# Performance work log

Hardware: AMD Instinct MI355X
Metric: run time of the kernel (lower is better)

Reference implementation:

```python
import jax, jax.numpy as jnp
import numpy as np

NTYPES = 2
B, N, MNEI = 4, 512, 100
M = MNEI * NTYPES          # neighbor slots = maxNeighborNum * ntypes
EMB_LAST = 100             # embedding net sizes [25, 50, 100]
FIT_H = 240
M2 = 16
RMIN, RMAX = 0.5, 6.0


def setup_inputs():
    key = jax.random.key(0)
    ks = jax.random.split(key, 24)
    r = jax.random.uniform(ks[0], (B, N, M), minval=0.6, maxval=7.0)
    v = jax.random.normal(ks[1], (B, N, M, 3))
    v = v / jnp.linalg.norm(v, axis=-1, keepdims=True)
    keep = jax.random.uniform(ks[2], (B, N, M)) < 0.7
    ImageDR = jnp.concatenate([r[..., None], r[..., None] * v], axis=-1)
    ImageDR = jnp.where(keep[..., None], ImageDR, 0.0).astype(jnp.float32)
    Imagetype_map = jax.random.randint(ks[3], (N,), 0, NTYPES)
    list_neigh = jax.random.randint(ks[4], (B, N, M), 0, N + 1)
    type_map = jnp.arange(NTYPES)
    davg = (0.01 * jax.random.normal(ks[5], (NTYPES, M, 4))).astype(jnp.float32)
    dstd = (1.0 + 0.1 * jax.random.uniform(ks[6], (NTYPES, M, 4))).astype(jnp.float32)

    def w(k, shape, fan):
        return (jax.random.normal(k, shape) / np.sqrt(fan)).astype(jnp.float32)

    def b(k, shape):
        return (0.1 * jax.random.normal(k, shape)).astype(jnp.float32)

    emb_W0 = w(ks[7], (NTYPES, NTYPES, 1, 25), 1)
    emb_b0 = b(ks[8], (NTYPES, NTYPES, 25))
    emb_W1 = w(ks[9], (NTYPES, NTYPES, 25, 50), 25)
    emb_b1 = b(ks[10], (NTYPES, NTYPES, 50))
    emb_W2 = w(ks[11], (NTYPES, NTYPES, 50, 100), 50)
    emb_b2 = b(ks[12], (NTYPES, NTYPES, 100))
    fin = M2 * EMB_LAST
    fit_W0 = w(ks[13], (NTYPES, fin, FIT_H), fin)
    fit_b0 = b(ks[14], (NTYPES, FIT_H))
    fit_W1 = w(ks[15], (NTYPES, FIT_H, FIT_H), FIT_H)
    fit_b1 = b(ks[16], (NTYPES, FIT_H))
    fit_W2 = w(ks[17], (NTYPES, FIT_H, FIT_H), FIT_H)
    fit_b2 = b(ks[18], (NTYPES, FIT_H))
    fit_W3 = w(ks[19], (NTYPES, FIT_H, 1), FIT_H)
    fit_b3 = b(ks[20], (NTYPES, 1))
    energy_shift = jnp.array([-3.37, -5.21], dtype=jnp.float32)
    return dict(list_neigh=list_neigh, Imagetype_map=Imagetype_map, type_map=type_map,
                ImageDR=ImageDR, nghost=0, davg=davg, dstd=dstd,
                emb_W0=emb_W0, emb_b0=emb_b0, emb_W1=emb_W1, emb_b1=emb_b1,
                emb_W2=emb_W2, emb_b2=emb_b2,
                fit_W0=fit_W0, fit_b0=fit_b0, fit_W1=fit_W1, fit_b1=fit_b1,
                fit_W2=fit_W2, fit_b2=fit_b2, fit_W3=fit_W3, fit_b3=fit_b3,
                energy_shift=energy_shift)


def _emb(s, W0, b0, W1, b1, W2, b2):
    # DeepPot-SE embedding net with doubling resnet connections
    h = jnp.tanh(s @ W0 + b0)                                   # [..., 25]
    h = jnp.tanh(h @ W1 + b1) + jnp.concatenate([h, h], -1)     # [..., 50]
    return jnp.tanh(h @ W2 + b2) + jnp.concatenate([h, h], -1)  # [..., 100]


def _fit(d, W0, b0, W1, b1, W2, b2, W3, b3):
    h = jnp.tanh(d @ W0 + b0)
    h = h + jnp.tanh(h @ W1 + b1)
    h = h + jnp.tanh(h @ W2 + b2)
    return h @ W3 + b3


def _forward(ImageDR, davg, dstd,
             emb_W0, emb_b0, emb_W1, emb_b1, emb_W2, emb_b2,
             fit_W0, fit_b0, fit_W1, fit_b1, fit_W2, fit_b2, fit_W3, fit_b3,
             energy_shift, Imagetype_map):
    Bsz, Nat, Mtot, _ = ImageDR.shape
    m = Mtot // NTYPES
    R = ImageDR[..., 0]
    Rsafe = jnp.where(R > 1e-5, R, 1.0)
    # smooth switching function s(r): 1/r below Rmin, polynomial taper to Rmax
    u = (R - RMIN) / (RMAX - RMIN)
    mid = (u ** 3 * (-6.0 * u * u + 15.0 * u - 10.0) + 1.0) / Rsafe
    S = jnp.where((R > 0) & (R < RMIN), 1.0 / Rsafe,
                  jnp.where((R > RMIN) & (R < RMAX), mid, 0.0))
    msk = (jnp.abs(R) > 1e-5)[..., None]
    Ri = jnp.concatenate([S[..., None],
                          jnp.where(msk, (S / Rsafe)[..., None] * ImageDR[..., 1:4], 0.0)],
                         axis=-1)                                    # [B,N,M,4] = (s, s*x/r, s*y/r, s*z/r)
    # per-center-type normalization (irregular gather of stats)
    Rn = (Ri - davg[Imagetype_map][None]) / dstd[Imagetype_map][None]
    tmask = [(Imagetype_map == i).astype(Rn.dtype)[None, :, None, None] for i in range(NTYPES)]
    xyz = jnp.zeros((Bsz, Nat, 4, EMB_LAST), Rn.dtype)
    for j in range(NTYPES):                                          # neighbor-type slice
        sl = Rn[:, :, j * m:(j + 1) * m, :]                          # [B,N,m,4]
        s = sl[..., 0:1]
        G = jnp.zeros(sl.shape[:3] + (EMB_LAST,), sl.dtype)
        for i in range(NTYPES):                                      # center type -> pair net (i, j)
            G = G + tmask[i] * _emb(s, emb_W0[i, j], emb_b0[i, j],
                                    emb_W1[i, j], emb_b1[i, j], emb_W2[i, j], emb_b2[i, j])
        xyz = xyz + jnp.einsum('bnmk,bnmc->bnkc', sl, G)
    xyz = xyz / (m * NTYPES)
    # descriptor D = (Ri^T G)^T (Ri^T G)[:, :M2], flattened -> [B,N,EMB_LAST*M2]
    D = jnp.einsum('bnkc,bnkd->bncd', xyz, xyz[..., :M2]).reshape(Bsz, Nat, -1)
    Ei = jnp.zeros((Bsz, Nat), D.dtype)
    for i in range(NTYPES):
        e = _fit(D, fit_W0[i], fit_b0[i], fit_W1[i], fit_b1[i],
                 fit_W2[i], fit_b2[i], fit_W3[i], fit_b3[i])[..., 0] + energy_shift[i]
        Ei = Ei + tmask[i][:, :, 0, 0] * e
    Etot = jnp.sum(Ei, axis=1)
    return Etot, Ei


def reference(list_neigh, Imagetype_map, type_map, ImageDR, nghost, davg, dstd,
              emb_W0, emb_b0, emb_W1, emb_b1, emb_W2, emb_b2,
              fit_W0, fit_b0, fit_W1, fit_b1, fit_W2, fit_b2, fit_W3, fit_b3,
              energy_shift):
    return _forward(ImageDR, davg, dstd,
                    emb_W0, emb_b0, emb_W1, emb_b1, emb_W2, emb_b2,
                    fit_W0, fit_b0, fit_W1, fit_b1, fit_W2, fit_b2, fit_W3, fit_b3,
                    energy_shift, Imagetype_map)
```

## Files before the change

### kernel.cpp

```cpp
#include <hip/hip_runtime.h>
#include <math.h>

#define NT 2
#define BSZ 4
#define NAT 512
#define NATOMS 2048
#define NNEI 200
#define EMB 100
#define FITH 240
#define DDIM 1600
#define TBK 1024

#define BIAS_F  16
#define W3C_F   (BIAS_F + 3 * 512)
#define PERM_I  2064
#define CNT_I   (PERM_I + 2064)
#define IPERM_I (CNT_I + 4)
#define USH_BYTE 24832
#define TBL_U   0
#define W0T_U   409600
#define W1T_U   (W0T_U + 819200)
#define W2T_U   (W1T_U + 262144)
#define D_U     (W2T_U + 262144)
#define D_SZ    (129 * 50 * 512)
#define USH_END (D_U + D_SZ)
#define WS_NEED ((size_t)USH_BYTE + (size_t)USH_END * 2)

#define N_W0 819200
#define N_W1 262144
#define N_W2 262144
#define N_B  1536
#define N_W3 512
#define N_EI 2048
#define N_WT (N_W0 + N_W1 + N_W2 + N_B + N_W3 + N_EI)
#define WT_BLK ((N_WT + 255) / 256)
#define TB_BLK 512

#define HPAD 264

typedef short s8v __attribute__((ext_vector_type(8)));
typedef float f4v __attribute__((ext_vector_type(4)));

__device__ __forceinline__ float ftanh(float x) {
    float ax = fabsf(x);
    float e = __expf(2.0f * ax);
    float t = 1.0f - __fdividef(2.0f, e + 1.0f);
    return (x < 0.0f) ? -t : t;
}
__device__ __forceinline__ unsigned short f2bf(float f) {
    unsigned u = __float_as_uint(f);
    u += 0x7FFFu + ((u >> 16) & 1u);
    return (unsigned short)(u >> 16);
}
__device__ __forceinline__ float bf2f(unsigned short s) {
    return __uint_as_float(((unsigned)s) << 16);
}
__device__ __forceinline__ float calc_S(float R) {
    float Rsafe = (R > 1e-5f) ? R : 1.0f;
    float u = (R - 0.5f) * (1.0f / 5.5f);
    float uu = u * u;
    float mid = (u * uu * (-6.0f * uu + 15.0f * u - 10.0f) + 1.0f) / Rsafe;
    float S = 0.0f;
    if (R > 0.0f && R < 0.5f)      S = 1.0f / Rsafe;
    else if (R > 0.5f && R < 6.0f) S = mid;
    return S;
}

__global__ void __launch_bounds__(256) prep_kernel(
    const float* __restrict__ fW0, const float* __restrict__ fW1,
    const float* __restrict__ fW2,
    const float* __restrict__ fb0, const float* __restrict__ fb1,
    const float* __restrict__ fb2,
    const float* __restrict__ fW3, const float* __restrict__ fb3,
    const float* __restrict__ eshift,
    const float* __restrict__ davg, const float* __restrict__ dstd,
    const float* __restrict__ eW0, const float* __restrict__ eb0,
    const float* __restrict__ eW1, const float* __restrict__ eb1,
    const float* __restrict__ eW2, const float* __restrict__ eb2,
    const int* __restrict__ itype,
    float* __restrict__ ws, float* __restrict__ out)
{
    __shared__ float los[100], his[100];
    __shared__ float rng[2];
    __shared__ float h0s[8][25];
    __shared__ float h1s[8][50];
    __shared__ int pcnt, poff0, poff1;
    const int tid = threadIdx.x;
    int bxg = blockIdx.x;
    unsigned short* u0 = (unsigned short*)((char*)ws + USH_BYTE);

    if (bxg < WT_BLK) {
        int id = bxg * 256 + tid;
        if (id < N_W0) {
            int e = id & 7, lane = (id >> 3) & 63;
            int rem = id >> 9;
            int kt = rem % 50, c16 = rem / 50;
            int n = c16 * 16 + (lane & 15);
            int k = kt * 32 + (lane >> 4) * 8 + e;
            float v = 0.0f;
            if (n < 240)                  v = fW0[(size_t)k * 240 + n];
            else if (n >= 256 && n < 496) v = fW0[(size_t)(1600 + k) * 240 + (n - 256)];
            u0[W0T_U + id] = f2bf(v);
            return;
        }
        id -= N_W0;
        if (id < N_W1) {
            int e = id & 7, lane = (id >> 3) & 63;
            int rem = id >> 9;
            int kt = rem & 15, c16 = rem >> 4;
            int n = c16 * 16 + (lane & 15);
            int k = kt * 32 + (lane >> 4) * 8 + e;
            float v = 0.0f;
            if (n < 240 && k < 240)       v = fW1[(size_t)k * 240 + n];
            else if (n >= 256 && n < 496 && k >= 256 && k < 496)
                                          v = fW1[(size_t)(240 + (k - 256)) * 240 + (n - 256)];
            u0[W1T_U + id] = f2bf(v);
            return;
        }
        id -= N_W1;
        if (id < N_W2) {
            int e = id & 7, lane = (id >> 3) & 63;
            int rem = id >> 9;
            int kt = rem & 15, c16 = rem >> 4;
            int n = c16 * 16 + (lane & 15);
            int k = kt * 32 + (lane >> 4) * 8 + e;
            float v = 0.0f;
            if (n < 240 && k < 240)       v = fW2[(size_t)k * 240 + n];
            else if (n >= 256 && n < 496 && k >= 256 && k < 496)
                                          v = fW2[(size_t)(240 + (k - 256)) * 240 + (n - 256)];
            u0[W2T_U + id] = f2bf(v);
            return;
        }
        id -= N_W2;
        if (id < N_B) {
            int l = id / 512, n = id - l * 512;
            const float* fb = (l == 0) ? fb0 : (l == 1) ? fb1 : fb2;
            float v = 0.0f;
            if (n < 240)                  v = fb[n];
            else if (n >= 256 && n < 496) v = fb[240 + (n - 256)];
            ws[BIAS_F + l * 512 + n] = v;
            return;
        }
        id -= N_B;
        if (id < N_W3) {
            int n = id;
            float v = 0.0f;
            if (n < 240)                  v = fW3[n];
            else if (n >= 256 && n < 496) v = fW3[240 + (n - 256)];
            ws[W3C_F + n] = v;
            return;
        }
        id -= N_W3;
        if (id < N_EI) {
            int t = itype[id & (NAT - 1)];
            out[4 + id] = fb3[t] + eshift[t];
        }
        return;
    }
    bxg -= WT_BLK;
    if (bxg < TB_BLK) {
        const int nid = bxg >> 7;
        const int kb  = (bxg & 127) * 8;
        const int t = nid >> 1, j = nid & 1;
        if (tid < 100) {
            int m = j * 100 + tid;
            float av = davg[(t * NNEI + m) * 4];
            float sd = dstd[(t * NNEI + m) * 4];
            float inv = __fdividef(1.0f, sd);
            float a = (0.0f - av) * inv;
            float b = (2.0f - av) * inv;
            los[tid] = fminf(a, b);
            his[tid] = fmaxf(a, b);
        }
        __syncthreads();
        if (tid == 0) {
            float lo = los[0], hi = his[0];
            for (int i = 1; i < 100; ++i) { lo = fminf(lo, los[i]); hi = fmaxf(hi, his[i]); }
            rng[0] = lo; rng[1] = hi - lo;
            if (kb == 0) {
                ws[nid * 2] = lo;
                ws[nid * 2 + 1] = (float)(TBK - 1) / (hi - lo);
            }
        }
        __syncthreads();
        const float smin = rng[0], span = rng[1];
        const float* W0 = eW0 + nid * 25;
        const float* B0 = eb0 + nid * 25;
        if (tid < 200) {
            int q = tid / 25, a = tid % 25;
            float s = smin + span * ((float)(kb + q) * (1.0f / (TBK - 1)));
            h0s[q][a] = ftanh(fmaf(s, W0[a], B0[a]));
        }
        __syncthreads();
        const float* W1 = eW1 + nid * 1250;
        const float* B1 = eb1 + nid * 50;
        for (int idx = tid; idx < 400; idx += 256) {
            int q = idx / 50, cc = idx % 50;
            float acc = B1[cc];
#pragma unroll
            for (int a = 0; a < 25; ++a) acc = fmaf(h0s[q][a], W1[a * 50 + cc], acc);
            h1s[q][cc] = ftanh(acc) + h0s[q][(cc < 25) ? cc : cc - 25];
        }
        __syncthreads();
        const float* W2 = eW2 + nid * 5000;
        const float* B2 = eb2 + nid * 100;
        unsigned short* tblu = u0 + TBL_U;
        for (int idx = tid; idx < 800; idx += 256) {
            int q = idx / 100, c = idx % 100;
            float acc = B2[c];
#pragma unroll
            for (int a = 0; a < 50; ++a) acc = fmaf(h1s[q][a], W2[a * 100 + c], acc);
            float g = ftanh(acc) + h1s[q][(c < 50) ? c : c - 50];
            tblu[(size_t)(nid * TBK + kb + q) * 100 + c] = f2bf(g);
        }
        return;
    }
    if (tid == 0) { pcnt = 0; poff0 = 0; poff1 = 0; }
    __syncthreads();
    int* wsi = (int*)ws;
    int local0 = 0;
    for (int i = tid; i < NATOMS; i += 256) local0 += (itype[i & (NAT - 1)] == 0);
    atomicAdd(&pcnt, local0);
    __syncthreads();
    const int c0 = pcnt;
    const int c0p = (c0 + 15) & ~15;
    for (int i = tid; i < NATOMS; i += 256) {
        int t = itype[i & (NAT - 1)];
        int pos = (t == 0) ? atomicAdd(&poff0, 1) : (c0p + atomicAdd(&poff1, 1));
        wsi[PERM_I + pos] = i;
        wsi[IPERM_I + i] = pos;
    }
    if (tid == 0) {
        wsi[CNT_I] = c0; wsi[CNT_I + 1] = NATOMS - c0; wsi[CNT_I + 2] = c0p;
    }
}

__global__ void __launch_bounds__(128) embed_kernel(
    const int* __restrict__ itype, const float* __restrict__ imagedr,
    const float* __restrict__ davg, const float* __restrict__ dstd,
    float* __restrict__ ws)
{
    __shared__ __align__(16) float4 srn[NNEI];
    __shared__ float sx[NNEI];
    __shared__ float part[2][400];
    const int atom = blockIdx.x;
    const int n = atom & (NAT - 1);
    const int tid = threadIdx.x;
    const int t = itype[n];
    unsigned short* u0 = (unsigned short*)((char*)ws + USH_BYTE);
    const int* wsi = (const int*)ws;

    const float sm0 = ws[(t * 2 + 0) * 2], sc0 = ws[(t * 2 + 0) * 2 + 1];
    const float sm1 = ws[(t * 2 + 1) * 2], sc1 = ws[(t * 2 + 1) * 2 + 1];

    for (int m = tid; m < NNEI; m += 128) {
        float4 dr = ((const float4*)imagedr)[(size_t)atom * NNEI + m];
        float R = dr.x;
        float S = calc_S(R);
        float Rsafe = (R > 1e-5f) ? R : 1.0f;
        float sr = (fabsf(R) > 1e-5f) ? (S / Rsafe) : 0.0f;
        float4 av = ((const float4*)davg)[t * NNEI + m];
        float4 sd = ((const float4*)dstd)[t * NNEI + m];
        float4 rv;
        rv.x = (S         - av.x) / sd.x;
        rv.y = (sr * dr.y - av.y) / sd.y;
        rv.z = (sr * dr.z - av.z) / sd.z;
        rv.w = (sr * dr.w - av.w) / sd.w;
        srn[m] = rv;
        float smin = (m >= 100) ? sm1 : sm0;
        float scal = (m >= 100) ? sc1 : sc0;
        sx[m] = fminf(fmaxf((rv.x - smin) * scal, 0.0f), (float)(TBK - 2) + 0.9999f);
    }
    __syncthreads();

    const int w = tid >> 6, lane = tid & 63;
    const unsigned short* T = u0 + TBL_U + (size_t)(t * 2 + w) * TBK * EMB;
    const bool hi = (lane < 36);
    float xA0 = 0, xA1 = 0, xA2 = 0, xA3 = 0;
    float xB0 = 0, xB1 = 0, xB2 = 0, xB3 = 0;
#pragma unroll 4
    for (int mi = 0; mi < 100; ++mi) {
        int m = w * 100 + mi;
        float4 rv = srn[m];
        float x = sx[m];
        int i = (int)x;
        float f = x - (float)i;
        const unsigned short* Tr = T + (size_t)i * EMB;
        float g0 = bf2f(Tr[lane]);
        float g1 = bf2f(Tr[EMB + lane]);
        float g = fmaf(f, g1 - g0, g0);
        xA0 = fmaf(rv.x, g, xA0); xA1 = fmaf(rv.y, g, xA1);
        xA2 = fmaf(rv.z, g, xA2); xA3 = fmaf(rv.w, g, xA3);
        if (hi) {
            float h0v = bf2f(Tr[64 + lane]);
            float h1v = bf2f(Tr[EMB + 64 + lane]);
            float g2 = fmaf(f, h1v - h0v, h0v);
            xB0 = fmaf(rv.x, g2, xB0); xB1 = fmaf(rv.y, g2, xB1);
            xB2 = fmaf(rv.z, g2, xB2); xB3 = fmaf(rv.w, g2, xB3);
        }
    }
    part[w][0 * 100 + lane] = xA0; part[w][1 * 100 + lane] = xA1;
    part[w][2 * 100 + lane] = xA2; part[w][3 * 100 + lane] = xA3;
    if (hi) {
        part[w][0 * 100 + 64 + lane] = xB0; part[w][1 * 100 + 64 + lane] = xB1;
        part[w][2 * 100 + 64 + lane] = xB2; part[w][3 * 100 + 64 + lane] = xB3;
    }
    __syncthreads();
    const float inv = 1.0f / 200.0f;
    for (int idx = tid; idx < 400; idx += 128)
        part[0][idx] = (part[0][idx] + part[1][idx]) * inv;
    __syncthreads();
    const int p = wsi[IPERM_I + atom];
    const int rb = p >> 4, mrp = p & 15;
    unsigned short* Df = u0 + D_U;
    const float* xt = part[0];
    for (int k8 = tid; k8 < 200; k8 += 128) {
        int k = k8 * 8;
        int c = k >> 4, d0 = k & 15;
        int kt = k >> 5, q = (k >> 3) & 3;
        s8v pack;
#pragma unroll
        for (int e = 0; e < 8; ++e) {
            int d = d0 + e;
            float s = xt[c] * xt[d] + xt[100 + c] * xt[100 + d]
                    + xt[200 + c] * xt[200 + d] + xt[300 + c] * xt[300 + d];
            ((unsigned short*)&pack)[e] = f2bf(s);
        }
        *(s8v*)(Df + ((size_t)(rb * 50 + kt) * 64 + q * 16 + mrp) * 8) = pack;
    }
}

__global__ void __launch_bounds__(512) fit_kernel(
    const unsigned short* __restrict__ Af,
    const unsigned short* __restrict__ W0F,
    const unsigned short* __restrict__ W1F,
    const unsigned short* __restrict__ W2F,
    const float* __restrict__ biases,
    const float* __restrict__ w3c,
    const int* __restrict__ wsi,
    float* __restrict__ out)
{
    __shared__ float lred[4][64][17];
    __shared__ unsigned short Hs0[16 * HPAD];
    __shared__ unsigned short Hs1[16 * HPAD];
    __shared__ float red2[16][4];

    const int z = blockIdx.y;
    const int cnt = wsi[CNT_I + z];
    const int my = blockIdx.x;
    if (my * 16 >= cnt) return;
    const int basep = z ? wsi[CNT_I + 2] : 0;
    const int tid = threadIdx.x;
    const int w = tid >> 6, lane = tid & 63;
    const int mr = lane & 15, q = lane >> 4;
    const int wc = w & 3, h = w >> 2;
    const int n0 = z * 256 + wc * 64;
    const int m0 = my * 16;
    const int rb = (basep >> 4) + my;
    const int c16b = z * 16 + wc * 4;

    f4v a0 = {0,0,0,0}, a1 = {0,0,0,0}, a2 = {0,0,0,0}, a3 = {0,0,0,0};
    {
        const unsigned short* Ap = Af  + ((size_t)(rb * 50 + h * 25) * 64 + lane) * 8;
        const unsigned short* Bp = W0F + ((size_t)(c16b * 50 + h * 25) * 64 + lane) * 8;
#pragma unroll 5
        for (int kt = 0; kt < 25; ++kt) {
            s8v av = *(const s8v*)(Ap + kt * 512);
            s8v b0 = *(const s8v*)(Bp + kt * 512);
            s8v b1 = *(const s8v*)(Bp + 25600 + kt * 512);
            s8v b2 = *(const s8v*)(Bp + 51200 + kt * 512);
            s8v b3 = *(const s8v*)(Bp + 76800 + kt * 512);
            a0 = __builtin_amdgcn_mfma_f32_16x16x32_bf16(av, b0, a0, 0, 0, 0);
            a1 = __builtin_amdgcn_mfma_f32_16x16x32_bf16(av, b1, a1, 0, 0, 0);
            a2 = __builtin_amdgcn_mfma_f32_16x16x32_bf16(av, b2, a2, 0, 0, 0);
            a3 = __builtin_amdgcn_mfma_f32_16x16x32_bf16(av, b3, a3, 0, 0, 0);
        }
    }
    if (h == 1) {
#pragma unroll
        for (int r = 0; r < 4; ++r) {
            lred[wc][lane][r]      = a0[r];
            lred[wc][lane][4 + r]  = a1[r];
            lred[wc][lane][8 + r]  = a2[r];
            lred[wc][lane][12 + r] = a3[r];
        }
    }
    __syncthreads();
    if (h == 0) {
#pragma unroll
        for (int j = 0; j < 4; ++j) {
            const float bv = biases[n0 + j * 16 + mr];
            f4v* ap = (j == 0) ? &a0 : (j == 1) ? &a1 : (j == 2) ? &a2 : &a3;
            const int col = wc * 64 + j * 16 + mr;
#pragma unroll
            for (int r = 0; r < 4; ++r) {
                float s = (*ap)[r] + lred[wc][lane][j * 4 + r] + bv;
                int row = q * 4 + r;
                Hs0[row * HPAD + col] = f2bf(ftanh(s));
            }
        }
    }
    __syncthreads();

    {
        const unsigned short* Bp = W1F + ((size_t)(c16b * 16 + z * 8 + h * 4) * 64 + lane) * 8;
        f4v ac[4] = {{0,0,0,0},{0,0,0,0},{0,0,0,0},{0,0,0,0}};
#pragma unroll
        for (int kt = 0; kt < 4; ++kt) {
            s8v av = *(const s8v*)((const char*)Hs0
                     + (size_t)mr * (HPAD * 2) + h * 256 + q * 16 + kt * 64);
            s8v b0 = *(const s8v*)(Bp + kt * 512);
            s8v b1 = *(const s8v*)(Bp + 8192 + kt * 512);
            s8v b2 = *(const s8v*)(Bp + 16384 + kt * 512);
            s8v b3 = *(const s8v*)(Bp + 24576 + kt * 512);
            ac[0] = __builtin_amdgcn_mfma_f32_16x16x32_bf16(av, b0, ac[0], 0, 0, 0);
            ac[1] = __builtin_amdgcn_mfma_f32_16x16x32_bf16(av, b1, ac[1], 0, 0, 0);
            ac[2] = __builtin_amdgcn_mfma_f32_16x16x32_bf16(av, b2, ac[2], 0, 0, 0);
            ac[3] = __builtin_amdgcn_mfma_f32_16x16x32_bf16(av, b3, ac[3], 0, 0, 0);
        }
        if (h == 1) {
#pragma unroll
            for (int j = 0; j < 4; ++j)
#pragma unroll
                for (int r = 0; r < 4; ++r) lred[wc][lane][j * 4 + r] = ac[j][r];
        }
        __syncthreads();
        if (h == 0) {
#pragma unroll
            for (int j = 0; j < 4; ++j) {
                const float bv = biases[512 + n0 + j * 16 + mr];
                const int col = wc * 64 + j * 16 + mr;
#pragma unroll
                for (int r = 0; r < 4; ++r) {
                    float s = ac[j][r] + lred[wc][lane][j * 4 + r] + bv;
                    int row = q * 4 + r;
                    float hv = bf2f(Hs0[row * HPAD + col]) + ftanh(s);
                    Hs1[row * HPAD + col] = f2bf(hv);
                }
            }
        }
        __syncthreads();
    }

    {
        const unsigned short* Bp = W2F + ((size_t)(c16b * 16 + z * 8 + h * 4) * 64 + lane) * 8;
        f4v ac[4] = {{0,0,0,0},{0,0,0,0},{0,0,0,0},{0,0,0,0}};
#pragma unroll
        for (int kt = 0; kt < 4; ++kt) {
            s8v av = *(const s8v*)((const char*)Hs1
                     + (size_t)mr * (HPAD * 2) + h * 256 + q * 16 + kt * 64);
            s8v b0 = *(const s8v*)(Bp + kt * 512);
            s8v b1 = *(const s8v*)(Bp + 8192 + kt * 512);
            s8v b2 = *(const s8v*)(Bp + 16384 + kt * 512);
            s8v b3 = *(const s8v*)(Bp + 24576 + kt * 512);
            ac[0] = __builtin_amdgcn_mfma_f32_16x16x32_bf16(av, b0, ac[0], 0, 0, 0);
            ac[1] = __builtin_amdgcn_mfma_f32_16x16x32_bf16(av, b1, ac[1], 0, 0, 0);
            ac[2] = __builtin_amdgcn_mfma_f32_16x16x32_bf16(av, b2, ac[2], 0, 0, 0);
            ac[3] = __builtin_amdgcn_mfma_f32_16x16x32_bf16(av, b3, ac[3], 0, 0, 0);
        }
        if (h == 1) {
#pragma unroll
            for (int j = 0; j < 4; ++j)
#pragma unroll
                for (int r = 0; r < 4; ++r) lred[wc][lane][j * 4 + r] = ac[j][r];
        }
        __syncthreads();
        if (h == 0) {
            float pr[4] = {0, 0, 0, 0};
#pragma unroll
            for (int j = 0; j < 4; ++j) {
                const int col = n0 + j * 16 + mr;
                const float bv = biases[1024 + col];
                const float wv = w3c[col];
                const int coll = wc * 64 + j * 16 + mr;
#pragma unroll
                for (int r = 0; r < 4; ++r) {
                    float s = ac[j][r] + lred[wc][lane][j * 4 + r] + bv;
                    int row = q * 4 + r;
                    float hv = bf2f(Hs1[row * HPAD + coll]) + ftanh(s);
                    pr[r] = fmaf(hv, wv, pr[r]);
                }
            }
#pragma unroll
            for (int r = 0; r < 4; ++r) {
                float p = pr[r];
                p += __shfl_xor(p, 1, 16);
                p += __shfl_xor(p, 2, 16);
                p += __shfl_xor(p, 4, 16);
                p += __shfl_xor(p, 8, 16);
                if (mr == 0) red2[q * 4 + r][wc] = p;
            }
        }
        __syncthreads();
        if (tid < 16 && m0 + tid < cnt) {
            const int orow = wsi[PERM_I + basep + m0 + tid];
            out[4 + orow] += red2[tid][0] + red2[tid][1] + red2[tid][2] + red2[tid][3];
        }
    }
}

__global__ void etot_kernel(float* __restrict__ out) {
    const int b = blockIdx.x;
    float s = 0.0f;
    for (int n = threadIdx.x; n < NAT; n += 256) s += out[4 + b * NAT + n];
#pragma unroll
    for (int off = 32; off > 0; off >>= 1) s += __shfl_down(s, off, 64);
    __shared__ float rr[4];
    if ((threadIdx.x & 63) == 0) rr[threadIdx.x >> 6] = s;
    __syncthreads();
    if (threadIdx.x == 0) out[b] = rr[0] + rr[1] + rr[2] + rr[3];
}

__global__ void dp_atom_kernel(
    const int* __restrict__ itype, const float* __restrict__ imagedr,
    const float* __restrict__ davg, const float* __restrict__ dstd,
    const float* __restrict__ eW0, const float* __restrict__ eb0,
    const float* __restrict__ eW1, const float* __restrict__ eb1,
    const float* __restrict__ eW2, const float* __restrict__ eb2,
    const float* __restrict__ fW0, const float* __restrict__ fb0,
    const float* __restrict__ fW1, const float* __restrict__ fb1,
    const float* __restrict__ fW2, const float* __restrict__ fb2,
    const float* __restrict__ fW3, const float* __restrict__ fb3,
    const float* __restrict__ eshift, float* __restrict__ out)
{
    __shared__ __align__(16) float4 rn4[NNEI];
    __shared__ __align__(16) float  xyz[4 * EMB];
    __shared__ __align__(16) float  h0s[100 * 25];
    __shared__ __align__(16) float  smem[100 * 52];
    const int atom = blockIdx.x;
    const int n = atom & (NAT - 1);
    const int tid = threadIdx.x;
    const int t = itype[n];
    for (int m = tid; m < NNEI; m += 256) {
        float4 dr = ((const float4*)imagedr)[(size_t)atom * NNEI + m];
        float R = dr.x;
        float S = calc_S(R);
        float Rsafe = (R > 1e-5f) ? R : 1.0f;
        float sr = (fabsf(R) > 1e-5f) ? (S / Rsafe) : 0.0f;
        float4 av = ((const float4*)davg)[t * NNEI + m];
        float4 sd = ((const float4*)dstd)[t * NNEI + m];
        float4 rv;
        rv.x = (S - av.x) / sd.x; rv.y = (sr * dr.y - av.y) / sd.y;
        rv.z = (sr * dr.z - av.z) / sd.z; rv.w = (sr * dr.w - av.w) / sd.w;
        rn4[m] = rv;
    }
    const int c = tid & 127; const int mh = tid >> 7;
    float xp0 = 0, xp1 = 0, xp2 = 0, xp3 = 0;
    for (int j = 0; j < NT; ++j) {
        const int wb = t * NT + j;
        const float* W0 = eW0 + wb * 25; const float* B0 = eb0 + wb * 25;
        const float* W1 = eW1 + wb * 1250; const float* B1 = eb1 + wb * 50;
        const float* W2 = eW2 + wb * 5000; const float* B2 = eb2 + wb * 100;
        __syncthreads();
        for (int idx = tid; idx < 2500; idx += 256) {
            int m = idx / 25, a = idx - m * 25;
            h0s[idx] = ftanh(fmaf(rn4[j * 100 + m].x, W0[a], B0[a]));
        }
        __syncthreads();
        for (int idx = tid; idx < 5000; idx += 256) {
            int m = idx / 50, cc = idx - m * 50;
            const float* h0m = h0s + m * 25;
            float acc = B1[cc];
#pragma unroll
            for (int a = 0; a < 25; ++a) acc = fmaf(h0m[a], W1[a * 50 + cc], acc);
            smem[m * 52 + cc] = ftanh(acc) + h0m[(cc < 25) ? cc : cc - 25];
        }
        for (int idx = tid; idx < 200; idx += 256)
            smem[(idx >> 1) * 52 + 50 + (idx & 1)] = 0.0f;
        __syncthreads();
        if (c < EMB) {
            float w2c[52];
#pragma unroll
            for (int a = 0; a < 50; ++a) w2c[a] = W2[a * EMB + c];
            w2c[50] = 0; w2c[51] = 0;
            const float bc = B2[c];
            const int sk = (c < 50) ? c : c - 50;
            for (int i = 0; i < 50; ++i) {
                int m = mh * 50 + i;
                const float* h1m = smem + m * 52;
                float acc = bc;
#pragma unroll
                for (int q = 0; q < 13; ++q) {
                    float4 hv = ((const float4*)h1m)[q];
                    acc = fmaf(hv.x, w2c[4 * q], acc); acc = fmaf(hv.y, w2c[4 * q + 1], acc);
                    acc = fmaf(hv.z, w2c[4 * q + 2], acc); acc = fmaf(hv.w, w2c[4 * q + 3], acc);
                }
                float g = ftanh(acc) + h1m[sk];
                float4 rm = rn4[j * 100 + m];
                xp0 = fmaf(rm.x, g, xp0); xp1 = fmaf(rm.y, g, xp1);
                xp2 = fmaf(rm.z, g, xp2); xp3 = fmaf(rm.w, g, xp3);
            }
        }
    }
    __syncthreads();
    const float inv = 1.0f / 200.0f;
    if (mh == 0 && c < EMB) {
        xyz[c] = xp0 * inv; xyz[EMB + c] = xp1 * inv;
        xyz[2 * EMB + c] = xp2 * inv; xyz[3 * EMB + c] = xp3 * inv;
    }
    __syncthreads();
    if (mh == 1 && c < EMB) {
        xyz[c] += xp0 * inv; xyz[EMB + c] += xp1 * inv;
        xyz[2 * EMB + c] += xp2 * inv; xyz[3 * EMB + c] += xp3 * inv;
    }
    __syncthreads();
    float* Dld = smem;
    for (int idx = tid; idx < DDIM; idx += 256) {
        int cc = idx >> 4, d = idx & 15;
        Dld[idx] = xyz[cc] * xyz[d] + xyz[EMB + cc] * xyz[EMB + d]
                 + xyz[2 * EMB + cc] * xyz[2 * EMB + d] + xyz[3 * EMB + cc] * xyz[3 * EMB + d];
    }
    __syncthreads();
    float* hA = smem + DDIM; float* hB = hA + FITH; float* h2 = hB + FITH; float* red = h2 + FITH;
    if (tid < FITH) {
        const float* W = fW0 + (size_t)t * DDIM * FITH;
        float acc = fb0[t * FITH + tid];
        for (int f = 0; f < DDIM; f += 4) {
            float4 dv = *(const float4*)(Dld + f);
            acc = fmaf(dv.x, W[f * FITH + tid], acc); acc = fmaf(dv.y, W[(f + 1) * FITH + tid], acc);
            acc = fmaf(dv.z, W[(f + 2) * FITH + tid], acc); acc = fmaf(dv.w, W[(f + 3) * FITH + tid], acc);
        }
        hA[tid] = ftanh(acc);
    }
    __syncthreads();
    if (tid < FITH) {
        const float* W = fW1 + t * FITH * FITH;
        float acc = fb1[t * FITH + tid];
        for (int f = 0; f < FITH; f += 4) {
            float4 hv = *(const float4*)(hA + f);
            acc = fmaf(hv.x, W[f * FITH + tid], acc); acc = fmaf(hv.y, W[(f + 1) * FITH + tid], acc);
            acc = fmaf(hv.z, W[(f + 2) * FITH + tid], acc); acc = fmaf(hv.w, W[(f + 3) * FITH + tid], acc);
        }
        hB[tid] = hA[tid] + ftanh(acc);
    }
    __syncthreads();
    if (tid < FITH) {
        const float* W = fW2 + t * FITH * FITH;
        float acc = fb2[t * FITH + tid];
        for (int f = 0; f < FITH; f += 4) {
            float4 hv = *(const float4*)(hB + f);
            acc = fmaf(hv.x, W[f * FITH + tid], acc); acc = fmaf(hv.y, W[(f + 1) * FITH + tid], acc);
            acc = fmaf(hv.z, W[(f + 2) * FITH + tid], acc); acc = fmaf(hv.w, W[(f + 3) * FITH + tid], acc);
        }
        h2[tid] = hB[tid] + ftanh(acc);
    }
    __syncthreads();
    float p = (tid < FITH) ? h2[tid] * fW3[t * FITH + tid] : 0.0f;
#pragma unroll
    for (int off = 32; off > 0; off >>= 1) p += __shfl_down(p, off, 64);
    if ((tid & 63) == 0) red[tid >> 6] = p;
    __syncthreads();
    if (tid == 0) out[4 + atom] = red[0] + red[1] + red[2] + red[3] + fb3[t] + eshift[t];
}

extern "C" void kernel_launch(void* const* d_in, const int* in_sizes, int n_in,
                              void* d_out, int out_size, void* d_ws, size_t ws_size,
                              hipStream_t stream) {
    const int*   itype   = (const int*)  d_in[1];
    const float* imagedr = (const float*)d_in[3];
    const float* davg    = (const float*)d_in[5];
    const float* dstd    = (const float*)d_in[6];
    const float* eW0     = (const float*)d_in[7];
    const float* eb0     = (const float*)d_in[8];
    const float* eW1     = (const float*)d_in[9];
    const float* eb1     = (const float*)d_in[10];
    const float* eW2     = (const float*)d_in[11];
    const float* eb2     = (const float*)d_in[12];
    const float* fW0     = (const float*)d_in[13];
    const float* fb0     = (const float*)d_in[14];
    const float* fW1     = (const float*)d_in[15];
    const float* fb1     = (const float*)d_in[16];
    const float* fW2     = (const float*)d_in[17];
    const float* fb2     = (const float*)d_in[18];
    const float* fW3     = (const float*)d_in[19];
    const float* fb3     = (const float*)d_in[20];
    const float* eshift  = (const float*)d_in[21];
    float* out = (float*)d_out;
    float* ws  = (float*)d_ws;

    if (ws_size >= WS_NEED) {
        unsigned short* u0 = (unsigned short*)((char*)ws + USH_BYTE);
        const int* wsi = (const int*)ws;
        prep_kernel<<<WT_BLK + TB_BLK + 1, 256, 0, stream>>>(
            fW0, fW1, fW2, fb0, fb1, fb2, fW3, fb3, eshift,
            davg, dstd, eW0, eb0, eW1, eb1, eW2, eb2, itype, ws, out);
        embed_kernel<<<NATOMS, 128, 0, stream>>>(itype, imagedr, davg, dstd, ws);
        fit_kernel<<<dim3(128, 2), 512, 0, stream>>>(
            u0 + D_U, u0 + W0T_U, u0 + W1T_U, u0 + W2T_U,
            ws + BIAS_F, ws + W3C_F, wsi, out);
        etot_kernel<<<BSZ, 256, 0, stream>>>(out);
    } else {
        dp_atom_kernel<<<NATOMS, 256, 0, stream>>>(itype, imagedr, davg, dstd,
            eW0, eb0, eW1, eb1, eW2, eb2,
            fW0, fb0, fW1, fb1, fW2, fb2, fW3, fb3, eshift, out);
        etot_kernel<<<BSZ, 256, 0, stream>>>(out);
    }
}
```

Baseline: 179.9 us.

## Fuse energy sum into fit kernel and split embed neighbor loop across four waves

The per-frame total-energy reduction now runs inside the fit kernel: the last block to finish, found through an atomic done counter, sums the per-atom energies, which removes the separate etot launch. The embed kernel goes from 128 to 256 threads, each wave covering half of one type's neighbors, with a four-way partial reduction in shared memory. The fit kernel also gets a min-blocks-per-CU launch bound of 2 and a fully unrolled layer-0 K loop. This saves one launch and raises parallelism in embed, at the cost of an atomic, threadfences and possible register pressure.

```diff
diff --git a/kernel.cpp b/kernel.cpp
--- a/kernel.cpp
+++ b/kernel.cpp
@@ -16,6 +16,7 @@
 #define PERM_I  2064
 #define CNT_I   (PERM_I + 2064)
 #define IPERM_I (CNT_I + 4)
+#define DONE_I  (IPERM_I + 2048)
 #define USH_BYTE 24832
 #define TBL_U   0
 #define W0T_U   409600
@@ -37,6 +38,7 @@
 #define TB_BLK 512
 
 #define HPAD 264
+#define FIT_NBLK 256
 
 typedef short s8v __attribute__((ext_vector_type(8)));
 typedef float f4v __attribute__((ext_vector_type(4)));
@@ -232,17 +234,18 @@
     }
     if (tid == 0) {
         wsi[CNT_I] = c0; wsi[CNT_I + 1] = NATOMS - c0; wsi[CNT_I + 2] = c0p;
-    }
-}
-
-__global__ void __launch_bounds__(128) embed_kernel(
+        wsi[DONE_I] = 0;
+    }
+}
+
+__global__ void __launch_bounds__(256) embed_kernel(
     const int* __restrict__ itype, const float* __restrict__ imagedr,
     const float* __restrict__ davg, const float* __restrict__ dstd,
     float* __restrict__ ws)
 {
     __shared__ __align__(16) float4 srn[NNEI];
     __shared__ float sx[NNEI];
-    __shared__ float part[2][400];
+    __shared__ float part[4][400];
     const int atom = blockIdx.x;
     const int n = atom & (NAT - 1);
     const int tid = threadIdx.x;
@@ -253,7 +256,7 @@
     const float sm0 = ws[(t * 2 + 0) * 2], sc0 = ws[(t * 2 + 0) * 2 + 1];
     const float sm1 = ws[(t * 2 + 1) * 2], sc1 = ws[(t * 2 + 1) * 2 + 1];
 
-    for (int m = tid; m < NNEI; m += 128) {
+    for (int m = tid; m < NNEI; m += 256) {
         float4 dr = ((const float4*)imagedr)[(size_t)atom * NNEI + m];
         float R = dr.x;
         float S = calc_S(R);
@@ -273,13 +276,15 @@
     }
     __syncthreads();
 
-    const int w = tid >> 6, lane = tid & 63;
+    const int v = tid >> 6, lane = tid & 63;
+    const int w = v >> 1;
+    const int seg = v & 1;
     const unsigned short* T = u0 + TBL_U + (size_t)(t * 2 + w) * TBK * EMB;
     const bool hi = (lane < 36);
     float xA0 = 0, xA1 = 0, xA2 = 0, xA3 = 0;
     float xB0 = 0, xB1 = 0, xB2 = 0, xB3 = 0;
-#pragma unroll 4
-    for (int mi = 0; mi < 100; ++mi) {
+#pragma unroll 5
+    for (int mi = seg * 50; mi < seg * 50 + 50; ++mi) {
         int m = w * 100 + mi;
         float4 rv = srn[m];
         float x = sx[m];
@@ -299,22 +304,22 @@
             xB2 = fmaf(rv.z, g2, xB2); xB3 = fmaf(rv.w, g2, xB3);
         }
     }
-    part[w][0 * 100 + lane] = xA0; part[w][1 * 100 + lane] = xA1;
-    part[w][2 * 100 + lane] = xA2; part[w][3 * 100 + lane] = xA3;
+    part[v][0 * 100 + lane] = xA0; part[v][1 * 100 + lane] = xA1;
+    part[v][2 * 100 + lane] = xA2; part[v][3 * 100 + lane] = xA3;
     if (hi) {
-        part[w][0 * 100 + 64 + lane] = xB0; part[w][1 * 100 + 64 + lane] = xB1;
-        part[w][2 * 100 + 64 + lane] = xB2; part[w][3 * 100 + 64 + lane] = xB3;
+        part[v][0 * 100 + 64 + lane] = xB0; part[v][1 * 100 + 64 + lane] = xB1;
+        part[v][2 * 100 + 64 + lane] = xB2; part[v][3 * 100 + 64 + lane] = xB3;
     }
     __syncthreads();
     const float inv = 1.0f / 200.0f;
-    for (int idx = tid; idx < 400; idx += 128)
-        part[0][idx] = (part[0][idx] + part[1][idx]) * inv;
+    for (int idx = tid; idx < 400; idx += 256)
+        part[0][idx] = (part[0][idx] + part[1][idx] + part[2][idx] + part[3][idx]) * inv;
     __syncthreads();
     const int p = wsi[IPERM_I + atom];
     const int rb = p >> 4, mrp = p & 15;
     unsigned short* Df = u0 + D_U;
     const float* xt = part[0];
-    for (int k8 = tid; k8 < 200; k8 += 128) {
+    for (int k8 = tid; k8 < 200; k8 += 256) {
         int k = k8 * 8;
         int c = k >> 4, d0 = k & 15;
         int kt = k >> 5, q = (k >> 3) & 3;
@@ -330,172 +335,195 @@
     }
 }
 
-__global__ void __launch_bounds__(512) fit_kernel(
+__global__ void __launch_bounds__(512, 2) fit_kernel(
     const unsigned short* __restrict__ Af,
     const unsigned short* __restrict__ W0F,
     const unsigned short* __restrict__ W1F,
     const unsigned short* __restrict__ W2F,
     const float* __restrict__ biases,
     const float* __restrict__ w3c,
-    const int* __restrict__ wsi,
+    int* __restrict__ wsi,
     float* __restrict__ out)
 {
     __shared__ float lred[4][64][17];
     __shared__ unsigned short Hs0[16 * HPAD];
     __shared__ unsigned short Hs1[16 * HPAD];
     __shared__ float red2[16][4];
+    __shared__ int lastFlag;
+    __shared__ float er[8];
 
     const int z = blockIdx.y;
     const int cnt = wsi[CNT_I + z];
     const int my = blockIdx.x;
-    if (my * 16 >= cnt) return;
-    const int basep = z ? wsi[CNT_I + 2] : 0;
     const int tid = threadIdx.x;
-    const int w = tid >> 6, lane = tid & 63;
-    const int mr = lane & 15, q = lane >> 4;
-    const int wc = w & 3, h = w >> 2;
-    const int n0 = z * 256 + wc * 64;
-    const int m0 = my * 16;
-    const int rb = (basep >> 4) + my;
-    const int c16b = z * 16 + wc * 4;
-
-    f4v a0 = {0,0,0,0}, a1 = {0,0,0,0}, a2 = {0,0,0,0}, a3 = {0,0,0,0};
-    {
-        const unsigned short* Ap = Af  + ((size_t)(rb * 50 + h * 25) * 64 + lane) * 8;
-        const unsigned short* Bp = W0F + ((size_t)(c16b * 50 + h * 25) * 64 + lane) * 8;
-#pragma unroll 5
-        for (int kt = 0; kt < 25; ++kt) {
-            s8v av = *(const s8v*)(Ap + kt * 512);
-            s8v b0 = *(const s8v*)(Bp + kt * 512);
-            s8v b1 = *(const s8v*)(Bp + 25600 + kt * 512);
-            s8v b2 = *(const s8v*)(Bp + 51200 + kt * 512);
-            s8v b3 = *(const s8v*)(Bp + 76800 + kt * 512);
-            a0 = __builtin_amdgcn_mfma_f32_16x16x32_bf16(av, b0, a0, 0, 0, 0);
-            a1 = __builtin_amdgcn_mfma_f32_16x16x32_bf16(av, b1, a1, 0, 0, 0);
-            a2 = __builtin_amdgcn_mfma_f32_16x16x32_bf16(av, b2, a2, 0, 0, 0);
-            a3 = __builtin_amdgcn_mfma_f32_16x16x32_bf16(av, b3, a3, 0, 0, 0);
-        }
-    }
-    if (h == 1) {
-#pragma unroll
-        for (int r = 0; r < 4; ++r) {
-            lred[wc][lane][r]      = a0[r];
-            lred[wc][lane][4 + r]  = a1[r];
-            lred[wc][lane][8 + r]  = a2[r];
-            lred[wc][lane][12 + r] = a3[r];
-        }
-    }
-    __syncthreads();
-    if (h == 0) {
-#pragma unroll
-        for (int j = 0; j < 4; ++j) {
-            const float bv = biases[n0 + j * 16 + mr];
-            f4v* ap = (j == 0) ? &a0 : (j == 1) ? &a1 : (j == 2) ? &a2 : &a3;
-            const int col = wc * 64 + j * 16 + mr;
+    const bool work = (my * 16 < cnt);
+    if (work) {
+        const int basep = z ? wsi[CNT_I + 2] : 0;
+        const int w = tid >> 6, lane = tid & 63;
+        const int mr = lane & 15, q = lane >> 4;
+        const int wc = w & 3, h = w >> 2;
+        const int n0 = z * 256 + wc * 64;
+        const int m0 = my * 16;
+        const int rb = (basep >> 4) + my;
+        const int c16b = z * 16 + wc * 4;
+
+        f4v a0 = {0,0,0,0}, a1 = {0,0,0,0}, a2 = {0,0,0,0}, a3 = {0,0,0,0};
+        {
+            const unsigned short* Ap = Af  + ((size_t)(rb * 50 + h * 25) * 64 + lane) * 8;
+            const unsigned short* Bp = W0F + ((size_t)(c16b * 50 + h * 25) * 64 + lane) * 8;
+#pragma unroll
+            for (int kt = 0; kt < 25; ++kt) {
+                s8v av = *(const s8v*)(Ap + kt * 512);
+                s8v b0 = *(const s8v*)(Bp + kt * 512);
+                s8v b1 = *(const s8v*)(Bp + 25600 + kt * 512);
+                s8v b2 = *(const s8v*)(Bp + 51200 + kt * 512);
+                s8v b3 = *(const s8v*)(Bp + 76800 + kt * 512);
+                a0 = __builtin_amdgcn_mfma_f32_16x16x32_bf16(av, b0, a0, 0, 0, 0);
+                a1 = __builtin_amdgcn_mfma_f32_16x16x32_bf16(av, b1, a1, 0, 0, 0);
+                a2 = __builtin_amdgcn_mfma_f32_16x16x32_bf16(av, b2, a2, 0, 0, 0);
+                a3 = __builtin_amdgcn_mfma_f32_16x16x32_bf16(av, b3, a3, 0, 0, 0);
+            }
+        }
+        if (h == 1) {
 #pragma unroll
             for (int r = 0; r < 4; ++r) {
-                float s = (*ap)[r] + lred[wc][lane][j * 4 + r] + bv;
-                int row = q * 4 + r;
-                Hs0[row * HPAD + col] = f2bf(ftanh(s));
-            }
-        }
-    }
-    __syncthreads();
-
-    {
-        const unsigned short* Bp = W1F + ((size_t)(c16b * 16 + z * 8 + h * 4) * 64 + lane) * 8;
-        f4v ac[4] = {{0,0,0,0},{0,0,0,0},{0,0,0,0},{0,0,0,0}};
-#pragma unroll
-        for (int kt = 0; kt < 4; ++kt) {
-            s8v av = *(const s8v*)((const char*)Hs0
-                     + (size_t)mr * (HPAD * 2) + h * 256 + q * 16 + kt * 64);
-            s8v b0 = *(const s8v*)(Bp + kt * 512);
-            s8v b1 = *(const s8v*)(Bp + 8192 + kt * 512);
-            s8v b2 = *(const s8v*)(Bp + 16384 + kt * 512);
-            s8v b3 = *(const s8v*)(Bp + 24576 + kt * 512);
-            ac[0] = __builtin_amdgcn_mfma_f32_16x16x32_bf16(av, b0, ac[0], 0, 0, 0);
-            ac[1] = __builtin_amdgcn_mfma_f32_16x16x32_bf16(av, b1, ac[1], 0, 0, 0);
-            ac[2] = __builtin_amdgcn_mfma_f32_16x16x32_bf16(av, b2, ac[2], 0, 0, 0);
-            ac[3] = __builtin_amdgcn_mfma_f32_16x16x32_bf16(av, b3, ac[3], 0, 0, 0);
-        }
-        if (h == 1) {
-#pragma unroll
-            for (int j = 0; j < 4; ++j)
-#pragma unroll
-                for (int r = 0; r < 4; ++r) lred[wc][lane][j * 4 + r] = ac[j][r];
+                lred[wc][lane][r]      = a0[r];
+                lred[wc][lane][4 + r]  = a1[r];
+                lred[wc][lane][8 + r]  = a2[r];
+                lred[wc][lane][12 + r] = a3[r];
+            }
         }
         __syncthreads();
         if (h == 0) {
 #pragma unroll
             for (int j = 0; j < 4; ++j) {
-                const float bv = biases[512 + n0 + j * 16 + mr];
+                const float bv = biases[n0 + j * 16 + mr];
+                f4v* ap = (j == 0) ? &a0 : (j == 1) ? &a1 : (j == 2) ? &a2 : &a3;
                 const int col = wc * 64 + j * 16 + mr;
 #pragma unroll
                 for (int r = 0; r < 4; ++r) {
-                    float s = ac[j][r] + lred[wc][lane][j * 4 + r] + bv;
+                    float s = (*ap)[r] + lred[wc][lane][j * 4 + r] + bv;
                     int row = q * 4 + r;
-                    float hv = bf2f(Hs0[row * HPAD + col]) + ftanh(s);
-                    Hs1[row * HPAD + col] = f2bf(hv);
+                    Hs0[row * HPAD + col] = f2bf(ftanh(s));
                 }
             }
         }
         __syncthreads();
-    }
-
-    {
-        const unsigned short* Bp = W2F + ((size_t)(c16b * 16 + z * 8 + h * 4) * 64 + lane) * 8;
-        f4v ac[4] = {{0,0,0,0},{0,0,0,0},{0,0,0,0},{0,0,0,0}};
-#pragma unroll
-        for (int kt = 0; kt < 4; ++kt) {
-            s8v av = *(const s8v*)((const char*)Hs1
-                     + (size_t)mr * (HPAD * 2) + h * 256 + q * 16 + kt * 64);
-            s8v b0 = *(const s8v*)(Bp + kt * 512);
-            s8v b1 = *(const s8v*)(Bp + 8192 + kt * 512);
-            s8v b2 = *(const s8v*)(Bp + 16384 + kt * 512);
-            s8v b3 = *(const s8v*)(Bp + 24576 + kt * 512);
-            ac[0] = __builtin_amdgcn_mfma_f32_16x16x32_bf16(av, b0, ac[0], 0, 0, 0);
-            ac[1] = __builtin_amdgcn_mfma_f32_16x16x32_bf16(av, b1, ac[1], 0, 0, 0);
-            ac[2] = __builtin_amdgcn_mfma_f32_16x16x32_bf16(av, b2, ac[2], 0, 0, 0);
-            ac[3] = __builtin_amdgcn_mfma_f32_16x16x32_bf16(av, b3, ac[3], 0, 0, 0);
-        }
-        if (h == 1) {
-#pragma unroll
-            for (int j = 0; j < 4; ++j)
-#pragma unroll
-                for (int r = 0; r < 4; ++r) lred[wc][lane][j * 4 + r] = ac[j][r];
-        }
-        __syncthreads();
-        if (h == 0) {
-            float pr[4] = {0, 0, 0, 0};
-#pragma unroll
-            for (int j = 0; j < 4; ++j) {
-                const int col = n0 + j * 16 + mr;
-                const float bv = biases[1024 + col];
-                const float wv = w3c[col];
-                const int coll = wc * 64 + j * 16 + mr;
+
+        {
+            const unsigned short* Bp = W1F + ((size_t)(c16b * 16 + z * 8 + h * 4) * 64 + lane) * 8;
+            f4v ac[4] = {{0,0,0,0},{0,0,0,0},{0,0,0,0},{0,0,0,0}};
+#pragma unroll
+            for (int kt = 0; kt < 4; ++kt) {
+                s8v av = *(const s8v*)((const char*)Hs0
+                         + (size_t)mr * (HPAD * 2) + h * 256 + q * 16 + kt * 64);
+                s8v b0 = *(const s8v*)(Bp + kt * 512);
+                s8v b1 = *(const s8v*)(Bp + 8192 + kt * 512);
+                s8v b2 = *(const s8v*)(Bp + 16384 + kt * 512);
+                s8v b3 = *(const s8v*)(Bp + 24576 + kt * 512);
+                ac[0] = __builtin_amdgcn_mfma_f32_16x16x32_bf16(av, b0, ac[0], 0, 0, 0);
+                ac[1] = __builtin_amdgcn_mfma_f32_16x16x32_bf16(av, b1, ac[1], 0, 0, 0);
+                ac[2] = __builtin_amdgcn_mfma_f32_16x16x32_bf16(av, b2, ac[2], 0, 0, 0);
+                ac[3] = __builtin_amdgcn_mfma_f32_16x16x32_bf16(av, b3, ac[3], 0, 0, 0);
+            }
+            if (h == 1) {
+#pragma unroll
+                for (int j = 0; j < 4; ++j)
+#pragma unroll
+                    for (int r = 0; r < 4; ++r) lred[wc][lane][j * 4 + r] = ac[j][r];
+            }
+            __syncthreads();
+            if (h == 0) {
+#pragma unroll
+                for (int j = 0; j < 4; ++j) {
+                    const float bv = biases[512 + n0 + j * 16 + mr];
+                    const int col = wc * 64 + j * 16 + mr;
+#pragma unroll
+                    for (int r = 0; r < 4; ++r) {
+                        float s = ac[j][r] + lred[wc][lane][j * 4 + r] + bv;
+                        int row = q * 4 + r;
+                        float hv = bf2f(Hs0[row * HPAD + col]) + ftanh(s);
+                        Hs1[row * HPAD + col] = f2bf(hv);
+                    }
+                }
+            }
+            __syncthreads();
+        }
+
+        {
+            const unsigned short* Bp = W2F + ((size_t)(c16b * 16 + z * 8 + h * 4) * 64 + lane) * 8;
+            f4v ac[4] = {{0,0,0,0},{0,0,0,0},{0,0,0,0},{0,0,0,0}};
+#pragma unroll
+            for (int kt = 0; kt < 4; ++kt) {
+                s8v av = *(const s8v*)((const char*)Hs1
+                         + (size_t)mr * (HPAD * 2) + h * 256 + q * 16 + kt * 64);
+                s8v b0 = *(const s8v*)(Bp + kt * 512);
+                s8v b1 = *(const s8v*)(Bp + 8192 + kt * 512);
+                s8v b2 = *(const s8v*)(Bp + 16384 + kt * 512);
+                s8v b3 = *(const s8v*)(Bp + 24576 + kt * 512);
+                ac[0] = __builtin_amdgcn_mfma_f32_16x16x32_bf16(av, b0, ac[0], 0, 0, 0);
+                ac[1] = __builtin_amdgcn_mfma_f32_16x16x32_bf16(av, b1, ac[1], 0, 0, 0);
+                ac[2] = __builtin_amdgcn_mfma_f32_16x16x32_bf16(av, b2, ac[2], 0, 0, 0);
+                ac[3] = __builtin_amdgcn_mfma_f32_16x16x32_bf16(av, b3, ac[3], 0, 0, 0);
+            }
+            if (h == 1) {
+#pragma unroll
+                for (int j = 0; j < 4; ++j)
+#pragma unroll
+                    for (int r = 0; r < 4; ++r) lred[wc][lane][j * 4 + r] = ac[j][r];
+            }
+            __syncthreads();
+            if (h == 0) {
+                float pr[4] = {0, 0, 0, 0};
+#pragma unroll
+                for (int j = 0; j < 4; ++j) {
+                    const int col = n0 + j * 16 + mr;
+                    const float bv = biases[1024 + col];
+                    const float wv = w3c[col];
+                    const int coll = wc * 64 + j * 16 + mr;
+#pragma unroll
+                    for (int r = 0; r < 4; ++r) {
+                        float s = ac[j][r] + lred[wc][lane][j * 4 + r] + bv;
+                        int row = q * 4 + r;
+                        float hv = bf2f(Hs1[row * HPAD + coll]) + ftanh(s);
+                        pr[r] = fmaf(hv, wv, pr[r]);
+                    }
+                }
 #pragma unroll
                 for (int r = 0; r < 4; ++r) {
-                    float s = ac[j][r] + lred[wc][lane][j * 4 + r] + bv;
-                    int row = q * 4 + r;
-                    float hv = bf2f(Hs1[row * HPAD + coll]) + ftanh(s);
-                    pr[r] = fmaf(hv, wv, pr[r]);
+                    float p = pr[r];
+                    p += __shfl_xor(p, 1, 16);
+                    p += __shfl_xor(p, 2, 16);
+                    p += __shfl_xor(p, 4, 16);
+                    p += __shfl_xor(p, 8, 16);
+                    if (mr == 0) red2[q * 4 + r][wc] = p;
                 }
             }
-#pragma unroll
-            for (int r = 0; r < 4; ++r) {
-                float p = pr[r];
-                p += __shfl_xor(p, 1, 16);
-                p += __shfl_xor(p, 2, 16);
-                p += __shfl_xor(p, 4, 16);
-                p += __shfl_xor(p, 8, 16);
-                if (mr == 0) red2[q * 4 + r][wc] = p;
-            }
-        }
-        __syncthreads();
-        if (tid < 16 && m0 + tid < cnt) {
-            const int orow = wsi[PERM_I + basep + m0 + tid];
-            out[4 + orow] += red2[tid][0] + red2[tid][1] + red2[tid][2] + red2[tid][3];
-        }
+            __syncthreads();
+            if (tid < 16 && m0 + tid < cnt) {
+                const int orow = wsi[PERM_I + basep + m0 + tid];
+                out[4 + orow] += red2[tid][0] + red2[tid][1] + red2[tid][2] + red2[tid][3];
+            }
+        }
+    }
+
+    __syncthreads();
+    if (tid == 0) {
+        __threadfence();
+        int prev = atomicAdd(&wsi[DONE_I], 1);
+        lastFlag = (prev == FIT_NBLK - 1);
+    }
+    __syncthreads();
+    if (lastFlag) {
+        __threadfence();
+        const int g = tid >> 7, l = tid & 127;
+        float s = 0.0f;
+        for (int nn = l; nn < NAT; nn += 128) s += out[4 + g * NAT + nn];
+#pragma unroll
+        for (int off = 32; off > 0; off >>= 1) s += __shfl_down(s, off, 64);
+        if ((l & 63) == 0) er[g * 2 + (l >> 6)] = s;
+        __syncthreads();
+        if (tid < 4) out[tid] = er[tid * 2] + er[tid * 2 + 1];
     }
 }
 
@@ -680,15 +708,14 @@
 
     if (ws_size >= WS_NEED) {
         unsigned short* u0 = (unsigned short*)((char*)ws + USH_BYTE);
-        const int* wsi = (const int*)ws;
+        int* wsi = (int*)ws;
         prep_kernel<<<WT_BLK + TB_BLK + 1, 256, 0, stream>>>(
             fW0, fW1, fW2, fb0, fb1, fb2, fW3, fb3, eshift,
             davg, dstd, eW0, eb0, eW1, eb1, eW2, eb2, itype, ws, out);
-        embed_kernel<<<NATOMS, 128, 0, stream>>>(itype, imagedr, davg, dstd, ws);
+        embed_kernel<<<NATOMS, 256, 0, stream>>>(itype, imagedr, davg, dstd, ws);
         fit_kernel<<<dim3(128, 2), 512, 0, stream>>>(
             u0 + D_U, u0 + W0T_U, u0 + W1T_U, u0 + W2T_U,
             ws + BIAS_F, ws + W3C_F, wsi, out);
-        etot_kernel<<<BSZ, 256, 0, stream>>>(out);
     } else {
         dp_atom_kernel<<<NATOMS, 256, 0, stream>>>(itype, imagedr, davg, dstd,
             eW0, eb0, eW1, eb1, eW2, eb2,
```

After: 168.4 us. 6.4% less time.
